# Performance work log

Hardware: AMD Instinct MI355X
Metric: run time of the kernel (lower is better)

The kernel has to match this reference:

```python
import jax, jax.numpy as jnp
import numpy as np

N_NODES = 50000
N_EDGES = 600000
DIMS = [128, 128, 128, 2]  # layer_sizes + out_dim


def _glorot(key, shape):
    fan_in, fan_out = shape
    lim = (6.0 / (fan_in + fan_out)) ** 0.5
    return jax.random.uniform(key, shape, jnp.float32, -lim, lim)


def setup_inputs() -> dict:
    key = jax.random.key(0)
    ks = jax.random.split(key, 3 + 3 * (len(DIMS) - 1))
    inp = {
        "x": jax.random.normal(ks[0], (N_NODES, DIMS[0]), jnp.float32),
        "src": jax.random.randint(ks[1], (N_EDGES,), 0, N_NODES, jnp.int32),
        "dst": jax.random.randint(ks[2], (N_EDGES,), 0, N_NODES, jnp.int32),
    }
    for l in range(len(DIMS) - 1):
        din, dout = DIMS[l], DIMS[l + 1]
        inp[f"Wself{l}"] = _glorot(ks[3 + 3 * l], (din, dout))
        inp[f"Wneigh{l}"] = _glorot(ks[4 + 3 * l], (din, dout))
        inp[f"b{l}"] = jnp.zeros((dout,), jnp.float32)
    return inp


def _sage_layer(h, src, dst, Wself, Wneigh, b):
    # gather src features, sum into dst, divide by clamped in-degree (DGL mean)
    agg = jax.ops.segment_sum(h[src], dst, num_segments=N_NODES)  # [N, d]
    deg = jax.ops.segment_sum(jnp.ones((src.shape[0],), h.dtype), dst,
                              num_segments=N_NODES)
    h_neigh = agg / jnp.maximum(deg, 1.0)[:, None]
    return h @ Wself + h_neigh @ Wneigh + b


def reference(x, src, dst, Wself0, Wneigh0, b0, Wself1, Wneigh1, b1,
              Wself2, Wneigh2, b2):
    params = [(Wself0, Wneigh0, b0), (Wself1, Wneigh1, b1), (Wself2, Wneigh2, b2)]
    h = x
    for ix, (Ws, Wn, b) in enumerate(params):
        if ix > 0:
            h = jax.nn.relu(h)
        h = _sage_layer(h, src, dst, Ws, Wn, b)
    return h  # [N, 2]
```

## Files before the change

kernel.cpp:

```cpp
#include <hip/hip_runtime.h>

#define D 128
#define KSTR 264
#define CAP 64
#define NXCD 8
#define PREP_BLOCKS 1024
#define FILL_BLOCKS 2048

typedef __attribute__((ext_vector_type(8))) short short8;
typedef __attribute__((ext_vector_type(4))) short short4v;
typedef __attribute__((ext_vector_type(4))) float f32x4;

__device__ inline unsigned short f2b(float f) {
    unsigned u = __float_as_uint(f);
    u += 0x7FFFu + ((u >> 16) & 1u);
    return (unsigned short)(u >> 16);
}
__device__ inline float b2f_lo(unsigned v) { return __uint_as_float(v << 16); }
__device__ inline float b2f_hi(unsigned v) { return __uint_as_float(v & 0xFFFF0000u); }


__global__ __launch_bounds__(256) void k_prep_fill(
        const float* __restrict__ x, unsigned short* __restrict__ xb, int nx8,
        const float* __restrict__ Ws0, const float* __restrict__ Wn0,
        const float* __restrict__ Ws1, const float* __restrict__ Wn1,
        unsigned short* __restrict__ WT0, unsigned short* __restrict__ WT1,
        const int* __restrict__ src, const int* __restrict__ dst,
        int* __restrict__ cnt, unsigned short* __restrict__ col,
        int E, int perXcd) {
    int bid = blockIdx.x;
    if (bid < PREP_BLOCKS) {
        int gsize = PREP_BLOCKS * 256;
        int g = bid * 256 + threadIdx.x;
        for (int it = g; it < nx8; it += gsize) {
            int i = it * 8;
            float4 a = *(const float4*)&x[i];
            float4 b = *(const float4*)&x[i + 4];
            short8 v;
            v[0] = (short)f2b(a.x); v[1] = (short)f2b(a.y);
            v[2] = (short)f2b(a.z); v[3] = (short)f2b(a.w);
            v[4] = (short)f2b(b.x); v[5] = (short)f2b(b.y);
            v[6] = (short)f2b(b.z); v[7] = (short)f2b(b.w);
            *(short8*)&xb[i] = v;
        }
        for (int idx = g; idx < 2 * 128 * 256; idx += gsize) {
            int layer = idx >> 15;
            int r = idx & 32767;
            int k = r >> 7;
            int nn = r & 127;
            const float* Ws = layer ? Ws1 : Ws0;
            const float* Wn = layer ? Wn1 : Wn0;
            unsigned short* Wt = layer ? WT1 : WT0;
            float v = (k < 128) ? Ws[k * 128 + nn] : Wn[(k - 128) * 128 + nn];
            Wt[nn * KSTR + k] = f2b(v);
        }
    } else {
        int fb = bid - PREP_BLOCKS;
        int owner = fb & (NXCD - 1);
        int group = fb >> 3;
        int nGroups = FILL_BLOCKS >> 3;
        int lo = owner * perXcd;
        int hi = lo + perXcd;
        int stride = nGroups * 256;
        for (int e = group * 256 + threadIdx.x; e < E; e += stride) {
            int d = dst[e];
            if (d >= lo && d < hi) {
                int p = atomicAdd(&cnt[d], 1);
                if (p < CAP) col[(size_t)d * CAP + p] = (unsigned short)src[e];
            }
        }
    }
}


__global__ __launch_bounds__(256) void k_agg_b(const unsigned short* __restrict__ h,
                                               const int* __restrict__ cnt,
                                               const unsigned short* __restrict__ col,
                                               unsigned short* __restrict__ hn, int N) {
    int w = (blockIdx.x * 256 + threadIdx.x) >> 6;
    int lane = threadIdx.x & 63;
    if (w >= N) return;
    int degT = cnt[w];
    int deg = min(degT, CAP);
    int myc = (lane < deg) ? (int)col[(size_t)w * CAP + lane] : 0;
    int half = lane >> 5;
    int fo = (lane & 31) * 4;
    float a0 = 0.f, a1 = 0.f, a2 = 0.f, a3 = 0.f;
    int j = 0;
    for (; j + 16 <= deg; j += 16) {
        uint2 v[8];
#pragma unroll
        for (int u = 0; u < 8; ++u) {
            int s = __shfl(myc, j + u * 2 + half);
            v[u] = *(const uint2*)&h[(size_t)s * D + fo];
        }
#pragma unroll
        for (int u = 0; u < 8; ++u) {
            a0 += b2f_lo(v[u].x); a1 += b2f_hi(v[u].x);
            a2 += b2f_lo(v[u].y); a3 += b2f_hi(v[u].y);
        }
    }
    for (; j + 8 <= deg; j += 8) {
        uint2 v[4];
#pragma unroll
        for (int u = 0; u < 4; ++u) {
            int s = __shfl(myc, j + u * 2 + half);
            v[u] = *(const uint2*)&h[(size_t)s * D + fo];
        }
#pragma unroll
        for (int u = 0; u < 4; ++u) {
            a0 += b2f_lo(v[u].x); a1 += b2f_hi(v[u].x);
            a2 += b2f_lo(v[u].y); a3 += b2f_hi(v[u].y);
        }
    }
    for (; j < deg; j += 2) {
        int rj = j + half;
        int s = __shfl(myc, min(rj, deg - 1));
        float m = (rj < deg) ? 1.f : 0.f;
        uint2 v = *(const uint2*)&h[(size_t)s * D + fo];
        a0 += m * b2f_lo(v.x); a1 += m * b2f_hi(v.x);
        a2 += m * b2f_lo(v.y); a3 += m * b2f_hi(v.y);
    }
    a0 += __shfl_xor(a0, 32); a1 += __shfl_xor(a1, 32);
    a2 += __shfl_xor(a2, 32); a3 += __shfl_xor(a3, 32);
    if (half == 0) {
        float inv = 1.0f / fmaxf((float)degT, 1.0f);
        uint2 o;
        o.x = (unsigned)f2b(a0 * inv) | ((unsigned)f2b(a1 * inv) << 16);
        o.y = (unsigned)f2b(a2 * inv) | ((unsigned)f2b(a3 * inv) << 16);
        *(uint2*)&hn[(size_t)w * D + fo] = o;
    }
}


__global__ __launch_bounds__(256, 2) void k_gemm2(
        const unsigned short* __restrict__ Ah,
        const unsigned short* __restrict__ An,
        const unsigned short* __restrict__ Wt,
        const float* __restrict__ bias,
        unsigned short* __restrict__ out_h,
        const float* __restrict__ Ws2,
        const float* __restrict__ Wn2,
        const float* __restrict__ b2,
        float* __restrict__ out_final,
        float* __restrict__ p,
        int N, int mode) {
    __shared__ unsigned short Wl[128 * KSTR];
    int tid = threadIdx.x;
    int lane = tid & 63;
    int wid = tid >> 6;
    int l15 = lane & 15;
    int kq = lane >> 4;
    int waveRow = blockIdx.x * 128 + wid * 32;
    int r0c = min(waveRow + l15, N - 1);
    int r1c = min(waveRow + 16 + l15, N - 1);

    short8 a0[8], a1[8];
#pragma unroll
    for (int s = 0; s < 8; ++s) {
        const unsigned short* A = (s < 4) ? Ah : An;
        int kk = (s & 3) * 32 + kq * 8;
        a0[s] = *(const short8*)&A[(size_t)r0c * D + kk];
        a1[s] = *(const short8*)&A[(size_t)r1c * D + kk];
    }

    for (int i = tid * 8; i < 128 * KSTR; i += 2048)
        *(short8*)&Wl[i] = *(const short8*)&Wt[i];

    f32x4 acc[2][8];
#pragma unroll
    for (int m = 0; m < 2; ++m)
#pragma unroll
        for (int r = 0; r < 8; ++r) acc[m][r] = (f32x4){0.f, 0.f, 0.f, 0.f};

    __syncthreads();

    const unsigned short* lb = &Wl[l15 * KSTR + kq * 8];
#pragma unroll
    for (int s = 0; s < 8; ++s) {
#pragma unroll
        for (int r = 0; r < 8; ++r) {
            short8 bv = *(const short8*)&lb[s * 32 + r * (16 * KSTR)];
            acc[0][r] = __builtin_amdgcn_mfma_f32_16x16x32_bf16(bv, a0[s], acc[0][r], 0, 0, 0);
            acc[1][r] = __builtin_amdgcn_mfma_f32_16x16x32_bf16(bv, a1[s], acc[1][r], 0, 0, 0);
        }
    }

    if (mode == 0) {
#pragma unroll
        for (int m = 0; m < 2; ++m) {
            int row = waveRow + m * 16 + l15;
            if (row < N) {
#pragma unroll
                for (int r = 0; r < 8; ++r) {
                    int c = r * 16 + kq * 4;
                    float4 bb = *(const float4*)&bias[c];
                    float v0 = fmaxf(acc[m][r][0] + bb.x, 0.f);
                    float v1 = fmaxf(acc[m][r][1] + bb.y, 0.f);
                    float v2 = fmaxf(acc[m][r][2] + bb.z, 0.f);
                    float v3 = fmaxf(acc[m][r][3] + bb.w, 0.f);
                    short4v o;
                    o[0] = (short)f2b(v0); o[1] = (short)f2b(v1);
                    o[2] = (short)f2b(v2); o[3] = (short)f2b(v3);
                    *(short4v*)&out_h[(size_t)row * D + c] = o;
                }
            }
        }
    } else {
#pragma unroll
        for (int m = 0; m < 2; ++m) {
            float s0 = 0.f, s1 = 0.f, q0 = 0.f, q1 = 0.f;
#pragma unroll
            for (int r = 0; r < 8; ++r) {
                int c = r * 16 + kq * 4;
                float4 bb = *(const float4*)&bias[c];
#pragma unroll
                for (int jj = 0; jj < 4; ++jj) {
                    float v = fmaxf(acc[m][r][jj] + ((const float*)&bb)[jj], 0.f);
                    float2 ws = *(const float2*)&Ws2[(c + jj) * 2];
                    float2 wn = *(const float2*)&Wn2[(c + jj) * 2];
                    s0 += v * ws.x; s1 += v * ws.y;
                    q0 += v * wn.x; q1 += v * wn.y;
                }
            }
            s0 += __shfl_xor(s0, 16); s1 += __shfl_xor(s1, 16);
            q0 += __shfl_xor(q0, 16); q1 += __shfl_xor(q1, 16);
            s0 += __shfl_xor(s0, 32); s1 += __shfl_xor(s1, 32);
            q0 += __shfl_xor(q0, 32); q1 += __shfl_xor(q1, 32);
            int row = waveRow + m * 16 + l15;
            if (kq == 0 && row < N) {
                out_final[row * 2 + 0] = s0 + b2[0];
                out_final[row * 2 + 1] = s1 + b2[1];
                p[row * 2 + 0] = q0;
                p[row * 2 + 1] = q1;
            }
        }
    }
}


__global__ __launch_bounds__(256) void k_l2agg(const float* __restrict__ p,
                                               const int* __restrict__ cnt,
                                               const unsigned short* __restrict__ col,
                                               float* __restrict__ out, int N) {
    int n = blockIdx.x * 256 + threadIdx.x;
    if (n >= N) return;
    int degT = cnt[n];
    int deg = min(degT, CAP);
    const unsigned short* c = &col[(size_t)n * CAP];
    float a0 = 0.f, a1 = 0.f;
    for (int j = 0; j < deg; ++j) {
        int s = c[j];
        float2 v = *(const float2*)&p[(size_t)s * 2];
        a0 += v.x;
        a1 += v.y;
    }
    float inv = 1.0f / fmaxf((float)degT, 1.0f);
    out[n * 2 + 0] += a0 * inv;
    out[n * 2 + 1] += a1 * inv;
}


extern "C" void kernel_launch(void* const* d_in, const int* in_sizes, int n_in,
                              void* d_out, int out_size, void* d_ws, size_t ws_size,
                              hipStream_t stream) {
    const float* x   = (const float*)d_in[0];
    const int*   src = (const int*)d_in[1];
    const int*   dst = (const int*)d_in[2];
    const float* Ws0 = (const float*)d_in[3];
    const float* Wn0 = (const float*)d_in[4];
    const float* b0  = (const float*)d_in[5];
    const float* Ws1 = (const float*)d_in[6];
    const float* Wn1 = (const float*)d_in[7];
    const float* b1  = (const float*)d_in[8];
    const float* Ws2 = (const float*)d_in[9];
    const float* Wn2 = (const float*)d_in[10];
    const float* b2  = (const float*)d_in[11];
    float* out = (float*)d_out;

    int N = in_sizes[0] / D;
    int E = in_sizes[1];
    size_t NB = (size_t)N * D;

    unsigned short* B0 = (unsigned short*)d_ws;
    unsigned short* B1 = B0 + NB;
    unsigned short* B2 = B1 + NB;
    unsigned short* WT0 = B2 + NB;
    unsigned short* WT1 = WT0 + 128 * KSTR;
    float* p = (float*)(WT1 + 128 * KSTR);
    int* cnt = (int*)(p + 2 * (size_t)N);
    unsigned short* col = (unsigned short*)(cnt + N);

    int nx8 = (int)(NB >> 3);
    int perXcd = (N + NXCD - 1) / NXCD;

    hipMemsetAsync(cnt, 0, (size_t)N * sizeof(int), stream);

    k_prep_fill<<<PREP_BLOCKS + FILL_BLOCKS, 256, 0, stream>>>(
        x, B0, nx8, Ws0, Wn0, Ws1, Wn1, WT0, WT1,
        src, dst, cnt, col, E, perXcd);

    int aggGrid  = (N * 64 + 255) / 256;
    int gemmGrid = (N + 127) / 128;

    k_agg_b<<<aggGrid, 256, 0, stream>>>(B0, cnt, col, B1, N);
    k_gemm2<<<gemmGrid, 256, 0, stream>>>(B0, B1, WT0, b0, B2,
                                          nullptr, nullptr, nullptr, nullptr, nullptr,
                                          N, 0);

    k_agg_b<<<aggGrid, 256, 0, stream>>>(B2, cnt, col, B1, N);
    k_gemm2<<<gemmGrid, 256, 0, stream>>>(B2, B1, WT1, b1, nullptr,
                                          Ws2, Wn2, b2, out, p,
                                          N, 1);

    k_l2agg<<<(N + 255) / 256, 256, 0, stream>>>(p, cnt, col, out, N);
}
```

Baseline: 131.6 us.

## Split neighbor aggregation into feature slices with sliced output layout

The aggregation kernel now splits the 128 features into four 32-wide slices. Each slice is handled by its own block, and the 4-block groups are interleaved, presumably so each XCD's L2 sees a narrower working set of gathered rows. Within a wave, 8 lanes cover the 32 features and 8 edge groups run in parallel, combined with a shuffle reduction. The aggregated output is written in a slice-major layout that the GEMM reads back. The cost is shorter, 64-byte gathers per row, more blocks, extra shuffle reduction steps, and a row-major requirement on N.

```diff
diff --git a/kernel.cpp b/kernel.cpp
--- a/kernel.cpp
+++ b/kernel.cpp
@@ -73,69 +73,67 @@
 }
 
 
-__global__ __launch_bounds__(256) void k_agg_b(const unsigned short* __restrict__ h,
+__global__ __launch_bounds__(256) void k_agg_s(const unsigned short* __restrict__ h,
                                                const int* __restrict__ cnt,
                                                const unsigned short* __restrict__ col,
-                                               unsigned short* __restrict__ hn, int N) {
-    int w = (blockIdx.x * 256 + threadIdx.x) >> 6;
+                                               unsigned short* __restrict__ hnt,
+                                               int N) {
+    int slice = blockIdx.x & 3;
+    int ng = blockIdx.x >> 2;
+    int wid = threadIdx.x >> 6;
     int lane = threadIdx.x & 63;
+    int w = ng * 4 + wid;
     if (w >= N) return;
     int degT = cnt[w];
     int deg = min(degT, CAP);
     int myc = (lane < deg) ? (int)col[(size_t)w * CAP + lane] : 0;
-    int half = lane >> 5;
-    int fo = (lane & 31) * 4;
+    int q = lane >> 3;
+    int fo = slice * 32 + (lane & 7) * 4;
     float a0 = 0.f, a1 = 0.f, a2 = 0.f, a3 = 0.f;
     int j = 0;
     for (; j + 16 <= deg; j += 16) {
-        uint2 v[8];
-#pragma unroll
-        for (int u = 0; u < 8; ++u) {
-            int s = __shfl(myc, j + u * 2 + half);
-            v[u] = *(const uint2*)&h[(size_t)s * D + fo];
-        }
-#pragma unroll
-        for (int u = 0; u < 8; ++u) {
-            a0 += b2f_lo(v[u].x); a1 += b2f_hi(v[u].x);
-            a2 += b2f_lo(v[u].y); a3 += b2f_hi(v[u].y);
-        }
+        int s0 = __shfl(myc, j + q);
+        int s1 = __shfl(myc, j + 8 + q);
+        uint2 v0 = *(const uint2*)&h[(size_t)s0 * D + fo];
+        uint2 v1 = *(const uint2*)&h[(size_t)s1 * D + fo];
+        a0 += b2f_lo(v0.x) + b2f_lo(v1.x);
+        a1 += b2f_hi(v0.x) + b2f_hi(v1.x);
+        a2 += b2f_lo(v0.y) + b2f_lo(v1.y);
+        a3 += b2f_hi(v0.y) + b2f_hi(v1.y);
     }
     for (; j + 8 <= deg; j += 8) {
-        uint2 v[4];
-#pragma unroll
-        for (int u = 0; u < 4; ++u) {
-            int s = __shfl(myc, j + u * 2 + half);
-            v[u] = *(const uint2*)&h[(size_t)s * D + fo];
-        }
-#pragma unroll
-        for (int u = 0; u < 4; ++u) {
-            a0 += b2f_lo(v[u].x); a1 += b2f_hi(v[u].x);
-            a2 += b2f_lo(v[u].y); a3 += b2f_hi(v[u].y);
-        }
-    }
-    for (; j < deg; j += 2) {
-        int rj = j + half;
-        int s = __shfl(myc, min(rj, deg - 1));
+        int s0 = __shfl(myc, j + q);
+        uint2 v0 = *(const uint2*)&h[(size_t)s0 * D + fo];
+        a0 += b2f_lo(v0.x); a1 += b2f_hi(v0.x);
+        a2 += b2f_lo(v0.y); a3 += b2f_hi(v0.y);
+    }
+    if (j < deg) {
+        int rj = j + q;
+        int s0 = __shfl(myc, min(rj, deg - 1));
         float m = (rj < deg) ? 1.f : 0.f;
-        uint2 v = *(const uint2*)&h[(size_t)s * D + fo];
-        a0 += m * b2f_lo(v.x); a1 += m * b2f_hi(v.x);
-        a2 += m * b2f_lo(v.y); a3 += m * b2f_hi(v.y);
-    }
-    a0 += __shfl_xor(a0, 32); a1 += __shfl_xor(a1, 32);
-    a2 += __shfl_xor(a2, 32); a3 += __shfl_xor(a3, 32);
-    if (half == 0) {
+        uint2 v0 = *(const uint2*)&h[(size_t)s0 * D + fo];
+        a0 += m * b2f_lo(v0.x); a1 += m * b2f_hi(v0.x);
+        a2 += m * b2f_lo(v0.y); a3 += m * b2f_hi(v0.y);
+    }
+    for (int off = 8; off < 64; off <<= 1) {
+        a0 += __shfl_xor(a0, off);
+        a1 += __shfl_xor(a1, off);
+        a2 += __shfl_xor(a2, off);
+        a3 += __shfl_xor(a3, off);
+    }
+    if (q == 0) {
         float inv = 1.0f / fmaxf((float)degT, 1.0f);
         uint2 o;
         o.x = (unsigned)f2b(a0 * inv) | ((unsigned)f2b(a1 * inv) << 16);
         o.y = (unsigned)f2b(a2 * inv) | ((unsigned)f2b(a3 * inv) << 16);
-        *(uint2*)&hn[(size_t)w * D + fo] = o;
+        *(uint2*)&hnt[((size_t)slice * N + w) * 32 + (lane & 7) * 4] = o;
     }
 }
 
 
 __global__ __launch_bounds__(256, 2) void k_gemm2(
         const unsigned short* __restrict__ Ah,
-        const unsigned short* __restrict__ An,
+        const unsigned short* __restrict__ hnt,
         const unsigned short* __restrict__ Wt,
         const float* __restrict__ bias,
         unsigned short* __restrict__ out_h,
@@ -158,10 +156,15 @@
     short8 a0[8], a1[8];
 #pragma unroll
     for (int s = 0; s < 8; ++s) {
-        const unsigned short* A = (s < 4) ? Ah : An;
-        int kk = (s & 3) * 32 + kq * 8;
-        a0[s] = *(const short8*)&A[(size_t)r0c * D + kk];
-        a1[s] = *(const short8*)&A[(size_t)r1c * D + kk];
+        if (s < 4) {
+            int kk = s * 32 + kq * 8;
+            a0[s] = *(const short8*)&Ah[(size_t)r0c * D + kk];
+            a1[s] = *(const short8*)&Ah[(size_t)r1c * D + kk];
+        } else {
+            size_t sb = (size_t)(s & 3) * N;
+            a0[s] = *(const short8*)&hnt[(sb + r0c) * 32 + kq * 8];
+            a1[s] = *(const short8*)&hnt[(sb + r1c) * 32 + kq * 8];
+        }
     }
 
     for (int i = tid * 8; i < 128 * KSTR; i += 2048)
@@ -300,15 +303,15 @@
         x, B0, nx8, Ws0, Wn0, Ws1, Wn1, WT0, WT1,
         src, dst, cnt, col, E, perXcd);
 
-    int aggGrid  = (N * 64 + 255) / 256;
+    int aggGrid  = ((N + 3) / 4) * 4;
     int gemmGrid = (N + 127) / 128;
 
-    k_agg_b<<<aggGrid, 256, 0, stream>>>(B0, cnt, col, B1, N);
+    k_agg_s<<<aggGrid, 256, 0, stream>>>(B0, cnt, col, B1, N);
     k_gemm2<<<gemmGrid, 256, 0, stream>>>(B0, B1, WT0, b0, B2,
                                           nullptr, nullptr, nullptr, nullptr, nullptr,
                                           N, 0);
 
-    k_agg_b<<<aggGrid, 256, 0, stream>>>(B2, cnt, col, B1, N);
+    k_agg_s<<<aggGrid, 256, 0, stream>>>(B2, cnt, col, B1, N);
     k_gemm2<<<gemmGrid, 256, 0, stream>>>(B2, B1, WT1, b1, nullptr,
                                           Ws2, Wn2, b2, out, p,
                                           N, 1);
```

Measured after the change: 200.2 us. 52.2% more time.
